# Kernel optimization log

Measured on AMD Instinct MI355X. Metric: run time of the kernel, lower is better.

## Reference

```python
import jax, jax.numpy as jnp
import numpy as np

EXTENTS = (1, 1, 1)
DIM = 256
HEADS = 8
DH = 32
INNER = HEADS * DH
SCALE = DH ** -0.5
NEG = -1e9


def _windows(t):
    """t: (B, S, H, W, C) -> (B, S, H, W, K, C) local 3D windows, K = prod(2e+1).
    Pads with zeros, window dims flattened in (s, h, w) order (matches unfold i j k)."""
    e = EXTENTS
    B, S, H, W, C = t.shape
    tp = jnp.pad(t, [(0, 0), (e[0], e[0]), (e[1], e[1]), (e[2], e[2]), (0, 0)])
    slabs = []
    for dz in range(2 * e[0] + 1):
        for dy in range(2 * e[1] + 1):
            for dx in range(2 * e[2] + 1):
                slabs.append(tp[:, dz:dz + S, dy:dy + H, dx:dx + W, :])
    return jnp.stack(slabs, axis=4)


def setup_inputs() -> dict:
    key = jax.random.key(0)
    ks = jax.random.split(key, 8)
    B, S, H, W = 2, 8, 32, 32
    scale_w = DIM ** -0.5
    return {
        "x": jax.random.normal(ks[0], (B, S, H, W, DIM), jnp.float32),
        "q": jax.random.normal(ks[1], (B, S, H, W, DIM), jnp.float32),
        "Wq": jax.random.normal(ks[2], (DIM, INNER), jnp.float32) * scale_w,
        "Wk": jax.random.normal(ks[3], (DIM, INNER), jnp.float32) * scale_w,
        "Wv": jax.random.normal(ks[4], (DIM, INNER), jnp.float32) * scale_w,
        "bv": jax.random.normal(ks[5], (INNER,), jnp.float32) * 0.02,
        "Wo": jax.random.normal(ks[6], (INNER, DIM), jnp.float32) * (INNER ** -0.5),
        "bo": jax.random.normal(ks[7], (DIM,), jnp.float32) * 0.02,
    }


def reference(x, q, Wq, Wk, Wv, bv, Wo, bo):
    B, S, H, W, _ = x.shape
    k = x @ Wk                      # (B,S,H,W,INNER)
    v = x @ Wv + bv
    qp = q @ Wq

    kw = _windows(k)                # (B,S,H,W,K,INNER)
    vw = _windows(v)
    K = kw.shape[4]

    # mask: True where window element falls on padding (out of bounds)
    valid = _windows(jnp.ones((1, S, H, W, 1), jnp.float32))[..., 0] > 0  # (1,S,H,W,K)
    mask = ~valid

    qh = qp.reshape(B, S, H, W, HEADS, DH)
    kh = kw.reshape(B, S, H, W, K, HEADS, DH)
    vh = vw.reshape(B, S, H, W, K, HEADS, DH)

    dots = jnp.einsum('bshwnd,bshwknd->bshwnk', qh, kh) * SCALE  # (B,S,H,W,HEADS,K)
    dots = jnp.where(mask[:, :, :, :, None, :], NEG, dots)
    attn = jax.nn.softmax(dots, axis=-1)
    out = jnp.einsum('bshwnk,bshwknd->bshwnd', attn, vh)
    out = out.reshape(B, S, H, W, INNER)
    return out @ Wo + bo            # (B,S,H,W,DIM)
```

## Files before the change

kernel.cpp:

```cpp
#include <hip/hip_runtime.h>
#include <hip/hip_bf16.h>
#include <math.h>

#define B_N 2
#define S_N 8
#define H_N 32
#define W_N 32
#define DIM_N 256
#define NPOS (B_N * S_N * H_N * W_N)
#define NP (NPOS * DIM_N)
#define SCALE_F 0.1767766952966369f

typedef __attribute__((ext_vector_type(8))) short bf16x8;
typedef __attribute__((ext_vector_type(4))) float f32x4;

__device__ __forceinline__ unsigned short f2b(float f) {
    __hip_bfloat16 h = __float2bfloat16(f);
    return __builtin_bit_cast(unsigned short, h);
}
__device__ __forceinline__ unsigned pk2(float a, float b) {
    return (unsigned)f2b(a) | ((unsigned)f2b(b) << 16);
}
__device__ __forceinline__ float bl(unsigned u) { return __uint_as_float(u << 16); }
__device__ __forceinline__ float bh(unsigned u) { return __uint_as_float(u & 0xffff0000u); }

__global__ __launch_bounds__(256)
void wtrans_kernel(const float* __restrict__ Wq, const float* __restrict__ Wk,
                   const float* __restrict__ Wv, const float* __restrict__ Wo,
                   unsigned short* __restrict__ wt)
{
    int mat = blockIdx.y;
    const float* W = (mat == 0) ? Wq : (mat == 1) ? Wk : (mat == 2) ? Wv : Wo;
    unsigned short* Wt = wt + (size_t)mat * 65536;
    int tile = blockIdx.x;
    int tk = tile >> 3, tn = tile & 7;
    __shared__ float t[32][33];
    int c = threadIdx.x & 31;
    int r0 = (threadIdx.x >> 5) * 4;
#pragma unroll
    for (int i = 0; i < 4; ++i)
        t[r0 + i][c] = W[(size_t)(tk * 32 + r0 + i) * 256 + tn * 32 + c];
    __syncthreads();
#pragma unroll
    for (int i = 0; i < 4; ++i)
        Wt[(size_t)(tn * 32 + r0 + i) * 256 + tk * 32 + c] = f2b(t[c][r0 + i]);
}

__global__ __launch_bounds__(256, 3)
void proj_mfma(const float* __restrict__ x, const float* __restrict__ q,
               const unsigned short* __restrict__ wt, const float* __restrict__ bv,
               unsigned short* __restrict__ qh, unsigned short* __restrict__ kh,
               unsigned short* __restrict__ vh)
{
    __shared__ unsigned short Al[128][72];
    __shared__ unsigned short Bl[128][64];

    const int bx = blockIdx.x;
    const int z = bx >> 8;
    const int rem = bx & 255;
    const int row0 = (rem >> 1) * 128;
    const int col0 = (rem & 1) * 128;
    const float* A = (z == 0) ? q : x;
    const unsigned short* Wtm = wt + (size_t)z * 65536;
    unsigned short* outp = (z == 0) ? qh : (z == 1) ? kh : vh;
    const float* bias = (z == 2) ? bv : nullptr;

    const int tid = threadIdx.x;
    const int lane = tid & 63;
    const int wid = tid >> 6;
    const int wr = wid >> 1, wc = wid & 1;
    const int l15 = lane & 15, l4 = lane >> 4;

    f32x4 acc[4][4];
#pragma unroll
    for (int m = 0; m < 4; ++m)
#pragma unroll
        for (int n = 0; n < 4; ++n) acc[m][n] = (f32x4){0.f, 0.f, 0.f, 0.f};

    for (int kt = 0; kt < DIM_N; kt += 64) {
#pragma unroll
        for (int i = 0; i < 4; ++i) {
            int c = wid * 4 + i;
            int o = c * 64 + lane;
            int row = o >> 3, u = o & 7;
            int lu = u ^ (row & 7);
            const unsigned short* g =
                &Wtm[(size_t)(col0 + row) * DIM_N + kt + lu * 8];
            __builtin_amdgcn_global_load_lds(
                (const __attribute__((address_space(1))) unsigned int*)g,
                (__attribute__((address_space(3))) unsigned int*)&Bl[c * 8][0],
                16, 0, 0);
        }
#pragma unroll
        for (int i = 0; i < 8; ++i) {
            int o = i * 256 + tid;
            int row = o >> 4, qq = o & 15;
            float4 f = *(const float4*)&A[(size_t)(row0 + row) * DIM_N + kt + qq * 4];
            uint2 v;
            v.x = pk2(f.x, f.y);
            v.y = pk2(f.z, f.w);
            *(uint2*)&Al[row][qq * 4] = v;
        }
        __syncthreads();
#pragma unroll
        for (int ks = 0; ks < 2; ++ks) {
            bf16x8 af[4], bfr[4];
#pragma unroll
            for (int m = 0; m < 4; ++m)
                af[m] = *(const bf16x8*)&Al[wr * 64 + m * 16 + l15][ks * 32 + l4 * 8];
#pragma unroll
            for (int n = 0; n < 4; ++n) {
                int row = wc * 64 + n * 16 + l15;
                int su = (ks * 4 + l4) ^ (row & 7);
                bfr[n] = *(const bf16x8*)&Bl[row][su * 8];
            }
#pragma unroll
            for (int m = 0; m < 4; ++m)
#pragma unroll
                for (int n = 0; n < 4; ++n)
                    acc[m][n] = __builtin_amdgcn_mfma_f32_16x16x32_bf16(
                        af[m], bfr[n], acc[m][n], 0, 0, 0);
        }
        __syncthreads();
    }

#pragma unroll
    for (int n = 0; n < 4; ++n) {
        int col = col0 + wc * 64 + n * 16 + l15;
        float bb = bias ? bias[col] : 0.f;
        int head = col >> 5, dh = col & 31;
#pragma unroll
        for (int m = 0; m < 4; ++m) {
#pragma unroll
            for (int rg = 0; rg < 4; ++rg) {
                int row = row0 + wr * 64 + m * 16 + l4 * 4 + rg;
                outp[((size_t)head * NPOS + row) * 32 + dh] =
                    f2b(acc[m][n][rg] + bb);
            }
        }
    }
}

__global__ __launch_bounds__(256, 2)
void attn_fused(const unsigned short* __restrict__ qh, const unsigned short* __restrict__ kh,
                const unsigned short* __restrict__ vh, const unsigned short* __restrict__ wt3,
                const float* __restrict__ bo, float* __restrict__ out)
{
    __shared__ unsigned short aol[32 * 256];
    __shared__ unsigned short Bl[256][72];

    int p = blockIdx.x;
    int bix = (p & 7) * 64 + (p >> 3);
    int h = bix & 31, s = (bix >> 5) & 7, b = bix >> 8;
    int n = threadIdx.x >> 5;
    int w = threadIdx.x & 31;

    size_t rowbase = (((size_t)b * S_N + s) * H_N + h) * W_N;
    size_t pos = rowbase + w;
    const unsigned short* qrow = qh + ((size_t)n * NPOS + pos) * 32;
    float qv[32];
#pragma unroll
    for (int j = 0; j < 4; ++j) {
        uint4 u = ((const uint4*)qrow)[j];
        qv[j * 8 + 0] = bl(u.x); qv[j * 8 + 1] = bh(u.x);
        qv[j * 8 + 2] = bl(u.y); qv[j * 8 + 3] = bh(u.y);
        qv[j * 8 + 4] = bl(u.z); qv[j * 8 + 5] = bh(u.z);
        qv[j * 8 + 6] = bl(u.w); qv[j * 8 + 7] = bh(u.w);
    }

    float dots[27];
#pragma unroll
    for (int dz = 0; dz < 3; ++dz)
#pragma unroll
        for (int dy = 0; dy < 3; ++dy) {
            int ns = s + dz - 1, nh = h + dy - 1;
            bool rowok = (unsigned)ns < S_N && (unsigned)nh < H_N;
            size_t rb = rowok ? ((((size_t)b * S_N + ns) * H_N + nh) * W_N)
                              : rowbase;
            const unsigned short* base = kh + ((size_t)n * NPOS + rb + w) * 32;
            uint4 kr[3][4];
#pragma unroll
            for (int dx = 0; dx < 3; ++dx) {
                const uint4* kp = (const uint4*)(base + (dx - 1) * 32);
#pragma unroll
                for (int j = 0; j < 4; ++j) kr[dx][j] = kp[j];
            }
#pragma unroll
            for (int dx = 0; dx < 3; ++dx) {
                float acc = 0.f;
#pragma unroll
                for (int j = 0; j < 4; ++j) {
                    uint4 u = kr[dx][j];
                    acc = fmaf(qv[j * 8 + 0], bl(u.x), acc);
                    acc = fmaf(qv[j * 8 + 1], bh(u.x), acc);
                    acc = fmaf(qv[j * 8 + 2], bl(u.y), acc);
                    acc = fmaf(qv[j * 8 + 3], bh(u.y), acc);
                    acc = fmaf(qv[j * 8 + 4], bl(u.z), acc);
                    acc = fmaf(qv[j * 8 + 5], bh(u.z), acc);
                    acc = fmaf(qv[j * 8 + 6], bl(u.w), acc);
                    acc = fmaf(qv[j * 8 + 7], bh(u.w), acc);
                }
                int nw = w + dx - 1;
                bool ok = rowok && (unsigned)nw < W_N;
                dots[(dz * 3 + dy) * 3 + dx] = ok ? acc * SCALE_F : -1e30f;
            }
        }

    float m = dots[0];
#pragma unroll
    for (int i = 1; i < 27; ++i) m = fmaxf(m, dots[i]);
    float den = 0.f;
#pragma unroll
    for (int i = 0; i < 27; ++i) {
        float p2 = __expf(dots[i] - m);
        dots[i] = p2;
        den += p2;
    }
    float inv = 1.f / den;

    float ov[32];
#pragma unroll
    for (int i = 0; i < 32; ++i) ov[i] = 0.f;
#pragma unroll
    for (int dz = 0; dz < 3; ++dz)
#pragma unroll
        for (int dy = 0; dy < 3; ++dy) {
            int ns = s + dz - 1, nh = h + dy - 1;
            bool rowok = (unsigned)ns < S_N && (unsigned)nh < H_N;
            size_t rb = rowok ? ((((size_t)b * S_N + ns) * H_N + nh) * W_N)
                              : rowbase;
            const unsigned short* base = vh + ((size_t)n * NPOS + rb + w) * 32;
            uint4 vr[3][4];
#pragma unroll
            for (int dx = 0; dx < 3; ++dx) {
                const uint4* vp = (const uint4*)(base + (dx - 1) * 32);
#pragma unroll
                for (int j = 0; j < 4; ++j) vr[dx][j] = vp[j];
            }
#pragma unroll
            for (int dx = 0; dx < 3; ++dx) {
                float pw = dots[(dz * 3 + dy) * 3 + dx];
#pragma unroll
                for (int j = 0; j < 4; ++j) {
                    uint4 u = vr[dx][j];
                    ov[j * 8 + 0] = fmaf(pw, bl(u.x), ov[j * 8 + 0]);
                    ov[j * 8 + 1] = fmaf(pw, bh(u.x), ov[j * 8 + 1]);
                    ov[j * 8 + 2] = fmaf(pw, bl(u.y), ov[j * 8 + 2]);
                    ov[j * 8 + 3] = fmaf(pw, bh(u.y), ov[j * 8 + 3]);
                    ov[j * 8 + 4] = fmaf(pw, bl(u.z), ov[j * 8 + 4]);
                    ov[j * 8 + 5] = fmaf(pw, bh(u.z), ov[j * 8 + 5]);
                    ov[j * 8 + 6] = fmaf(pw, bl(u.w), ov[j * 8 + 6]);
                    ov[j * 8 + 7] = fmaf(pw, bh(u.w), ov[j * 8 + 7]);
                }
            }
        }

#pragma unroll
    for (int j = 0; j < 4; ++j) {
        uint4 o;
        o.x = pk2(ov[j * 8 + 0] * inv, ov[j * 8 + 1] * inv);
        o.y = pk2(ov[j * 8 + 2] * inv, ov[j * 8 + 3] * inv);
        o.z = pk2(ov[j * 8 + 4] * inv, ov[j * 8 + 5] * inv);
        o.w = pk2(ov[j * 8 + 6] * inv, ov[j * 8 + 7] * inv);
        int unit = n * 4 + j;
        int su = unit ^ (w & 7);
        *(uint4*)&aol[w * 256 + su * 8] = o;
    }

    const int lane = threadIdx.x & 63;
    const int wv = threadIdx.x >> 6;
    const int l15 = lane & 15, l4 = lane >> 4;

    f32x4 acc[2][4];
#pragma unroll
    for (int m2 = 0; m2 < 2; ++m2)
#pragma unroll
        for (int n2 = 0; n2 < 4; ++n2) acc[m2][n2] = (f32x4){0.f, 0.f, 0.f, 0.f};

    for (int kt = 0; kt < 4; ++kt) {
        __syncthreads();
#pragma unroll
        for (int i = 0; i < 8; ++i) {
            int u = threadIdx.x + i * 256;
            int rowb = u >> 3, su = u & 7;
            *(uint4*)&Bl[rowb][su * 8] =
                *(const uint4*)&wt3[(size_t)rowb * DIM_N + kt * 64 + su * 8];
        }
        __syncthreads();
#pragma unroll
        for (int ks = 0; ks < 2; ++ks) {
            bf16x8 af[2], bfr[4];
#pragma unroll
            for (int m2 = 0; m2 < 2; ++m2) {
                int r = m2 * 16 + l15;
                int unit = kt * 8 + ks * 4 + l4;
                int su = unit ^ (r & 7);
                af[m2] = *(const bf16x8*)&aol[r * 256 + su * 8];
            }
#pragma unroll
            for (int n2 = 0; n2 < 4; ++n2)
                bfr[n2] = *(const bf16x8*)&Bl[wv * 64 + n2 * 16 + l15][ks * 32 + l4 * 8];
#pragma unroll
            for (int m2 = 0; m2 < 2; ++m2)
#pragma unroll
                for (int n2 = 0; n2 < 4; ++n2)
                    acc[m2][n2] = __builtin_amdgcn_mfma_f32_16x16x32_bf16(
                        af[m2], bfr[n2], acc[m2][n2], 0, 0, 0);
        }
    }

#pragma unroll
    for (int n2 = 0; n2 < 4; ++n2) {
        int col = wv * 64 + n2 * 16 + l15;
        float bb = bo[col];
#pragma unroll
        for (int m2 = 0; m2 < 2; ++m2) {
#pragma unroll
            for (int rg = 0; rg < 4; ++rg) {
                int row = m2 * 16 + l4 * 4 + rg;
                out[(rowbase + row) * DIM_N + col] = acc[m2][n2][rg] + bb;
            }
        }
    }
}

extern "C" void kernel_launch(void* const* d_in, const int* in_sizes, int n_in,
                              void* d_out, int out_size, void* d_ws, size_t ws_size,
                              hipStream_t stream)
{
    const float* xin = (const float*)d_in[0];
    const float* qin = (const float*)d_in[1];
    const float* Wq  = (const float*)d_in[2];
    const float* Wk  = (const float*)d_in[3];
    const float* Wv  = (const float*)d_in[4];
    const float* bv  = (const float*)d_in[5];
    const float* Wo  = (const float*)d_in[6];
    const float* bo  = (const float*)d_in[7];
    float* out = (float*)d_out;

    unsigned short* ws = (unsigned short*)d_ws;
    unsigned short* wt = ws;
    unsigned short* qh = wt + (size_t)4 * 65536;
    unsigned short* kh = qh + (size_t)NP;
    unsigned short* vh = kh + (size_t)NP;

    dim3 gw(64, 4);
    wtrans_kernel<<<gw, 256, 0, stream>>>(Wq, Wk, Wv, Wo, wt);

    proj_mfma<<<768, 256, 0, stream>>>(xin, qin, wt, bv, qh, kh, vh);

    attn_fused<<<B_N * S_N * H_N, 256, 0, stream>>>(qh, kh, vh, wt + 3 * 65536, bo, out);
}
```

Before: 62.10 us.

## Fuse K and V projections per block and widen tile to full output width

The projection kernel now uses 512-thread blocks that each cover 64 rows across all 256 output columns. Blocks working on x compute both K and V from one shared A tile in LDS. Previously x was read and converted to bf16 separately for K and V and for each column half, so this cuts redundant fp32 input traffic and conversion work. In exchange, per-block LDS use rises to about 73KB, which limits occupancy. Q blocks do only half the MFMA work of KV blocks, so the load is unbalanced.

Result: slower. 64.83 us (+4.4%).

```diff
diff --git a/kernel.cpp b/kernel.cpp
--- a/kernel.cpp
+++ b/kernel.cpp
@@ -46,36 +46,36 @@
         Wt[(size_t)(tn * 32 + r0 + i) * 256 + tk * 32 + c] = f2b(t[c][r0 + i]);
 }
 
-__global__ __launch_bounds__(256, 3)
+__global__ __launch_bounds__(512, 2)
 void proj_mfma(const float* __restrict__ x, const float* __restrict__ q,
                const unsigned short* __restrict__ wt, const float* __restrict__ bv,
                unsigned short* __restrict__ qh, unsigned short* __restrict__ kh,
                unsigned short* __restrict__ vh)
 {
-    __shared__ unsigned short Al[128][72];
-    __shared__ unsigned short Bl[128][64];
+    __shared__ unsigned short Al[64][72];
+    __shared__ unsigned short Bl[2][256][64];
 
     const int bx = blockIdx.x;
-    const int z = bx >> 8;
-    const int rem = bx & 255;
-    const int row0 = (rem >> 1) * 128;
-    const int col0 = (rem & 1) * 128;
-    const float* A = (z == 0) ? q : x;
-    const unsigned short* Wtm = wt + (size_t)z * 65536;
-    unsigned short* outp = (z == 0) ? qh : (z == 1) ? kh : vh;
-    const float* bias = (z == 2) ? bv : nullptr;
+    const bool is_kv = bx >= 256;
+    const int row0 = (bx & 255) * 64;
+    const float* A = is_kv ? x : q;
+    const unsigned short* W0 = wt + (size_t)(is_kv ? 1 : 0) * 65536;
+    const unsigned short* W1 = wt + (size_t)2 * 65536;
 
     const int tid = threadIdx.x;
     const int lane = tid & 63;
     const int wid = tid >> 6;
-    const int wr = wid >> 1, wc = wid & 1;
+    const int wr = wid >> 2, wn = wid & 3;
     const int l15 = lane & 15, l4 = lane >> 4;
 
-    f32x4 acc[4][4];
-#pragma unroll
-    for (int m = 0; m < 4; ++m)
-#pragma unroll
-        for (int n = 0; n < 4; ++n) acc[m][n] = (f32x4){0.f, 0.f, 0.f, 0.f};
+    f32x4 accK[2][4], accV[2][4];
+#pragma unroll
+    for (int m = 0; m < 2; ++m)
+#pragma unroll
+        for (int n = 0; n < 4; ++n) {
+            accK[m][n] = (f32x4){0.f, 0.f, 0.f, 0.f};
+            accV[m][n] = (f32x4){0.f, 0.f, 0.f, 0.f};
+        }
 
     for (int kt = 0; kt < DIM_N; kt += 64) {
 #pragma unroll
@@ -84,16 +84,22 @@
             int o = c * 64 + lane;
             int row = o >> 3, u = o & 7;
             int lu = u ^ (row & 7);
-            const unsigned short* g =
-                &Wtm[(size_t)(col0 + row) * DIM_N + kt + lu * 8];
+            const unsigned short* g0 = &W0[(size_t)row * DIM_N + kt + lu * 8];
             __builtin_amdgcn_global_load_lds(
-                (const __attribute__((address_space(1))) unsigned int*)g,
-                (__attribute__((address_space(3))) unsigned int*)&Bl[c * 8][0],
+                (const __attribute__((address_space(1))) unsigned int*)g0,
+                (__attribute__((address_space(3))) unsigned int*)&Bl[0][c * 8][0],
                 16, 0, 0);
-        }
-#pragma unroll
-        for (int i = 0; i < 8; ++i) {
-            int o = i * 256 + tid;
+            if (is_kv) {
+                const unsigned short* g1 = &W1[(size_t)row * DIM_N + kt + lu * 8];
+                __builtin_amdgcn_global_load_lds(
+                    (const __attribute__((address_space(1))) unsigned int*)g1,
+                    (__attribute__((address_space(3))) unsigned int*)&Bl[1][c * 8][0],
+                    16, 0, 0);
+            }
+        }
+#pragma unroll
+        for (int i = 0; i < 2; ++i) {
+            int o = i * 512 + tid;
             int row = o >> 4, qq = o & 15;
             float4 f = *(const float4*)&A[(size_t)(row0 + row) * DIM_N + kt + qq * 4];
             uint2 v;
@@ -104,38 +110,61 @@
         __syncthreads();
 #pragma unroll
         for (int ks = 0; ks < 2; ++ks) {
-            bf16x8 af[4], bfr[4];
-#pragma unroll
-            for (int m = 0; m < 4; ++m)
-                af[m] = *(const bf16x8*)&Al[wr * 64 + m * 16 + l15][ks * 32 + l4 * 8];
-#pragma unroll
-            for (int n = 0; n < 4; ++n) {
-                int row = wc * 64 + n * 16 + l15;
-                int su = (ks * 4 + l4) ^ (row & 7);
-                bfr[n] = *(const bf16x8*)&Bl[row][su * 8];
-            }
-#pragma unroll
-            for (int m = 0; m < 4; ++m)
-#pragma unroll
-                for (int n = 0; n < 4; ++n)
-                    acc[m][n] = __builtin_amdgcn_mfma_f32_16x16x32_bf16(
-                        af[m], bfr[n], acc[m][n], 0, 0, 0);
+            bf16x8 af[2];
+#pragma unroll
+            for (int m = 0; m < 2; ++m)
+                af[m] = *(const bf16x8*)&Al[wr * 32 + m * 16 + l15][ks * 32 + l4 * 8];
+            {
+                bf16x8 b0[4];
+#pragma unroll
+                for (int n = 0; n < 4; ++n) {
+                    int row = wn * 64 + n * 16 + l15;
+                    int su = (ks * 4 + l4) ^ (row & 7);
+                    b0[n] = *(const bf16x8*)&Bl[0][row][su * 8];
+                }
+#pragma unroll
+                for (int m = 0; m < 2; ++m)
+#pragma unroll
+                    for (int n = 0; n < 4; ++n)
+                        accK[m][n] = __builtin_amdgcn_mfma_f32_16x16x32_bf16(
+                            af[m], b0[n], accK[m][n], 0, 0, 0);
+            }
+            if (is_kv) {
+                bf16x8 b1[4];
+#pragma unroll
+                for (int n = 0; n < 4; ++n) {
+                    int row = wn * 64 + n * 16 + l15;
+                    int su = (ks * 4 + l4) ^ (row & 7);
+                    b1[n] = *(const bf16x8*)&Bl[1][row][su * 8];
+                }
+#pragma unroll
+                for (int m = 0; m < 2; ++m)
+#pragma unroll
+                    for (int n = 0; n < 4; ++n)
+                        accV[m][n] = __builtin_amdgcn_mfma_f32_16x16x32_bf16(
+                            af[m], b1[n], accV[m][n], 0, 0, 0);
+            }
         }
         __syncthreads();
     }
 
 #pragma unroll
     for (int n = 0; n < 4; ++n) {
-        int col = col0 + wc * 64 + n * 16 + l15;
-        float bb = bias ? bias[col] : 0.f;
+        int col = wn * 64 + n * 16 + l15;
         int head = col >> 5, dh = col & 31;
-#pragma unroll
-        for (int m = 0; m < 4; ++m) {
+        float bb = is_kv ? bv[col] : 0.f;
+#pragma unroll
+        for (int m = 0; m < 2; ++m) {
 #pragma unroll
             for (int rg = 0; rg < 4; ++rg) {
-                int row = row0 + wr * 64 + m * 16 + l4 * 4 + rg;
-                outp[((size_t)head * NPOS + row) * 32 + dh] =
-                    f2b(acc[m][n][rg] + bb);
+                int row = row0 + wr * 32 + m * 16 + l4 * 4 + rg;
+                size_t off = ((size_t)head * NPOS + row) * 32 + dh;
+                if (is_kv) {
+                    kh[off] = f2b(accK[m][n][rg]);
+                    vh[off] = f2b(accV[m][n][rg] + bb);
+                } else {
+                    qh[off] = f2b(accK[m][n][rg]);
+                }
             }
         }
     }
@@ -347,7 +376,7 @@
     dim3 gw(64, 4);
     wtrans_kernel<<<gw, 256, 0, stream>>>(Wq, Wk, Wv, Wo, wt);
 
-    proj_mfma<<<768, 256, 0, stream>>>(xin, qin, wt, bv, qh, kh, vh);
+    proj_mfma<<<512, 512, 0, stream>>>(xin, qin, wt, bv, qh, kh, vh);
 
     attn_fused<<<B_N * S_N * H_N, 256, 0, stream>>>(qh, kh, vh, wt + 3 * 65536, bo, out);
 }
```
